# Kernel optimization log

Hardware: AMD Instinct MI355X
Metric: run time of the kernel (lower is better)

The kernel has to match this reference:

```python
import jax, jax.numpy as jnp
import numpy as np

# dims
N, NPG, E, D, ED = 32768, 256, 262144, 128, 32   # nodes, nodes/graph, edges, hidden, edge_dim
HG, CG = 4, 32                                    # GAT heads, per-head channels (HG*CG == D)
HA = 8                                            # global attention heads
DH = D // HA


def _glorot(key, shape):
    fan_in, fan_out = shape[0], shape[-1]
    lim = (6.0 / (fan_in + fan_out)) ** 0.5
    return jax.random.uniform(key, shape, jnp.float32, -lim, lim)


def _ln(x, g, b, eps=1e-5):
    m = x.mean(-1, keepdims=True)
    v = ((x - m) ** 2).mean(-1, keepdims=True)
    return (x - m) * jax.lax.rsqrt(v + eps) * g + b


def setup_inputs() -> dict:
    key = jax.random.key(0)
    ks = jax.random.split(key, 32)
    x = jax.random.normal(ks[0], (N, D), jnp.float32)
    src = jax.random.randint(ks[1], (E,), 0, N, jnp.int32)
    # keep edges intra-graph (graphs are contiguous blocks of NPG nodes)
    dst = (src // NPG) * NPG + jax.random.randint(ks[2], (E,), 0, NPG, jnp.int32)
    edge_index = jnp.stack([src, dst])
    edge_attr = jax.random.normal(ks[3], (E, ED), jnp.float32)
    batch = (jnp.arange(N, dtype=jnp.int32) // NPG)
    return {
        "x": x, "edge_attr": edge_attr,
        # EdgeAwareGATv2 params
        "W_src": _glorot(ks[4], (D, HG * CG)), "W_dst": _glorot(ks[5], (D, HG * CG)),
        "W_edge": _glorot(ks[6], (ED, HG * CG)), "att": _glorot(ks[7], (1, HG, CG)),
        "gat_bias": jnp.zeros((HG * CG,), jnp.float32),
        # GraphMultiHeadAttention params
        "Wq": _glorot(ks[8], (D, D)), "bq": jnp.zeros((D,), jnp.float32),
        "Wk": _glorot(ks[9], (D, D)), "bk": jnp.zeros((D,), jnp.float32),
        "Wv": _glorot(ks[10], (D, D)), "bv": jnp.zeros((D,), jnp.float32),
        "Wo": _glorot(ks[11], (D, D)), "bo": jnp.zeros((D,), jnp.float32),
        "We": _glorot(ks[12], (ED, HA)), "be": jnp.zeros((HA,), jnp.float32),
        # block norms + FFN
        "ln1_g": jnp.ones((D,), jnp.float32), "ln1_b": jnp.zeros((D,), jnp.float32),
        "W1": _glorot(ks[13], (D, 2 * D)), "b1": jnp.zeros((2 * D,), jnp.float32),
        "W2": _glorot(ks[14], (2 * D, D)), "b2": jnp.zeros((D,), jnp.float32),
        "ln2_g": jnp.ones((D,), jnp.float32), "ln2_b": jnp.zeros((D,), jnp.float32),
        "edge_index": edge_index, "batch": batch, "nodes_per_graph": NPG,
    }


def reference(x, edge_attr, W_src, W_dst, W_edge, att, gat_bias,
              Wq, bq, Wk, bk, Wv, bv, Wo, bo, We, be,
              ln1_g, ln1_b, W1, b1, W2, b2, ln2_g, ln2_b,
              edge_index, batch, nodes_per_graph):
    n = int(nodes_per_graph)
    Nn = x.shape[0]
    G = Nn // n
    src, dst = edge_index[0], edge_index[1]

    # ---- local: EdgeAwareGATv2 (segment-softmax attention over incoming edges) ----
    xs = (x @ W_src).reshape(Nn, HG, CG)
    xd = (x @ W_dst).reshape(Nn, HG, CG)
    ef = (edge_attr @ W_edge).reshape(-1, HG, CG)
    msg = jnp.tanh(xs[src] + xd[dst] + ef)                 # [E,HG,CG]
    alpha = (msg * att).sum(-1)                            # [E,HG]
    amax = jax.ops.segment_max(alpha, dst, num_segments=Nn)
    amax = jnp.where(jnp.isfinite(amax), amax, 0.0)        # nodes w/o in-edges
    ex = jnp.exp(alpha - amax[dst])
    den = jax.ops.segment_sum(ex, dst, num_segments=Nn)
    a = ex / (den[dst] + 1e-16)
    h_local = jax.ops.segment_sum(xs[src] * a[:, :, None], dst, num_segments=Nn)
    h_local = h_local.reshape(Nn, HG * CG) + gat_bias

    # ---- global: GraphMultiHeadAttention with edge bias (dense per graph) ----
    q = (x @ Wq + bq).reshape(G, n, HA, DH)
    k = (x @ Wk + bk).reshape(G, n, HA, DH)
    v = (x @ Wv + bv).reshape(G, n, HA, DH)
    attn = jnp.einsum('gnhd,gmhd->gnmh', q, k) * (DH ** -0.5)
    eb = edge_attr @ We + be                               # [E,HA]
    g_id = src // n
    intra = (g_id == dst // n)[:, None]
    attn = attn.at[g_id, src % n, dst % n].add(jnp.where(intra, eb, 0.0))
    attn = jax.nn.softmax(attn, axis=2)                    # softmax over keys (torch dim=1)
    h_attn = jnp.einsum('gnmh,gmhd->gnhd', attn, v).reshape(Nn, D)
    h_attn = h_attn @ Wo + bo

    # ---- GPS combine: residual + norm + FFN ----
    h = _ln(x + h_local + h_attn, ln1_g, ln1_b)
    ffn = jax.nn.gelu(h @ W1 + b1, approximate=False) @ W2 + b2
    return _ln(h + ffn, ln2_g, ln2_b)
```

## Files before the change

### kernel.cpp

```cpp
#include <hip/hip_runtime.h>
#include <hip/hip_bf16.h>

typedef __hip_bfloat16 bf16;
typedef __hip_bfloat162 bf162;
typedef __attribute__((ext_vector_type(8))) short short8;
typedef __attribute__((ext_vector_type(4))) float f32x4;
typedef __attribute__((ext_vector_type(16))) float f32x16;

constexpr int kN   = 32768;
constexpr int kG   = 128;
constexpr int kE   = 262144;
constexpr int kHA  = 8;

__device__ __forceinline__ float b2f(bf16 v){ return __bfloat162float(v); }
__device__ __forceinline__ bf16  f2b(float v){ return __float2bfloat16(v); }
__device__ __forceinline__ float b2f_raw(unsigned short u){
  return __uint_as_float((unsigned)u << 16);
}
__device__ __forceinline__ float tanh_fast(float x){
  float e = __expf(2.f*x);
  return 1.f - 2.f/(e+1.f);
}
__device__ __forceinline__ unsigned int cvtpk_bf16(float lo, float hi){
  unsigned int r;
  asm volatile("v_cvt_pk_bf16_f32 %0, %1, %2" : "=v"(r) : "v"(lo), "v"(hi));
  return r;
}
__device__ __forceinline__ void plane_swap(unsigned int &a, unsigned int &b){
  asm volatile("v_permlane32_swap_b32 %0, %1" : "+v"(a), "+v"(b));
}

__global__ void detect_k(const void* xraw, int* flag){
  const bf16* p = (const bf16*)xraw;
  int good = 0;
  for (int i = threadIdx.x; i < 4096; i += 256){
    float v = fabsf(b2f(p[i]));
    if (v > 0.0009765625f && v < 16.f) good++;
  }
  __shared__ int s[256];
  s[threadIdx.x] = good;
  __syncthreads();
  for (int d = 128; d; d >>= 1){
    if (threadIdx.x < d) s[threadIdx.x] += s[threadIdx.x + d];
    __syncthreads();
  }
  if (threadIdx.x == 0) *flag = (s[0] < 3500) ? 1 : 0;
}

struct ImpEnt { const void* src; void* dst; int n; };
struct ImpArgs { ImpEnt e[23]; };
__global__ __launch_bounds__(256) void import_k(ImpArgs a, const int* __restrict__ flag){
  ImpEnt en = a.e[blockIdx.y];
  const bool f32 = (*flag != 0);
  for (int i = blockIdx.x*256 + threadIdx.x; i < en.n; i += gridDim.x*256){
    float v = f32 ? ((const float*)en.src)[i] : b2f(((const bf16*)en.src)[i]);
    ((float*)en.dst)[i] = v;
  }
}

__global__ __launch_bounds__(256) void repack5_k(const float* __restrict__ W0,
    const float* __restrict__ W1p, const float* __restrict__ W2p,
    const float* __restrict__ W3p, const float* __restrict__ W4p,
    bf16* __restrict__ dst){
  int idx = blockIdx.x*256 + threadIdx.x;
  const float* Ws[5] = {W0, W1p, W2p, W3p, W4p};
  int o = idx >> 14;
  int rem = idx & 16383;
  int j = rem & 7, l = (rem >> 3) & 63, t = rem >> 9;
  int ks = t >> 3, cb = t & 7;
  int k = ks*32 + (l>>4)*8 + j;
  int c = cb*16 + (l&15);
  dst[idx] = f2b(Ws[o][k*128 + c]);
}

struct RepEnt { const float* src; bf16* dst; int total; int ncb_log; int dout; int perm; };
__global__ __launch_bounds__(256) void repack_k(RepEnt e0, RepEnt e1, RepEnt e2, RepEnt e3){
  RepEnt en = (blockIdx.y == 0) ? e0 : (blockIdx.y == 1) ? e1 :
              (blockIdx.y == 2) ? e2 : e3;
  int idx = blockIdx.x*256 + threadIdx.x;
  if (idx >= en.total) return;
  int j = idx & 7, l = (idx >> 3) & 63, t = idx >> 9;
  int ncbm = (1 << en.ncb_log) - 1;
  int ks = t >> en.ncb_log, cb = t & ncbm;
  int k = ks*32 + (l>>4)*8 + j;
  int c = cb*16 + (l&15);
  if (en.perm) c = ((c & 15) << 3) | (c >> 4);
  en.dst[idx] = f2b(en.src[k*en.dout + c]);
}

__global__ __launch_bounds__(256) void gemm5_k(const void* __restrict__ xraw,
    const int* __restrict__ flag,
    const bf16* __restrict__ Wrep, const float* __restrict__ bias5,
    bf16* __restrict__ proj5){
  const int tid = threadIdx.x;
  const int wid = tid >> 6, l = tid & 63;
  const long r0 = (long)blockIdx.x*64 + wid*16;
  const bool f32 = (*flag != 0);
  short8 af[4];
  if (f32){
    const float* fr = (const float*)xraw + (r0 + (l&15))*128;
    #pragma unroll
    for (int ks=0; ks<4; ks++){
      float4 a = *(const float4*)(fr + ks*32 + (l>>4)*8);
      float4 b = *(const float4*)(fr + ks*32 + (l>>4)*8 + 4);
      union{ unsigned int u[4]; short8 s; } c;
      c.u[0]=cvtpk_bf16(a.x,a.y); c.u[1]=cvtpk_bf16(a.z,a.w);
      c.u[2]=cvtpk_bf16(b.x,b.y); c.u[3]=cvtpk_bf16(b.z,b.w);
      af[ks] = c.s;
    }
  } else {
    const short* Arow = (const short*)xraw + (r0 + (l&15))*128;
    #pragma unroll
    for (int ks=0; ks<4; ks++)
      af[ks] = *(const short8*)(Arow + ks*32 + (l>>4)*8);
  }
  const short8* Wp = (const short8*)Wrep;
  const int cc = l & 15, rr = (l >> 4) * 4;
  #pragma unroll 1
  for (int o=0; o<5; o++){
    f32x4 acc[8];
    #pragma unroll
    for (int cb=0; cb<8; cb++) acc[cb] = (f32x4){0.f,0.f,0.f,0.f};
    #pragma unroll
    for (int ks=0; ks<4; ks++){
      #pragma unroll
      for (int cb=0; cb<8; cb++){
        short8 bf = Wp[(o*32 + ks*8 + cb)*64 + l];
        acc[cb] = __builtin_amdgcn_mfma_f32_16x16x32_bf16(af[ks], bf, acc[cb], 0,0,0);
      }
    }
    bf16* outb = proj5 + (long)o*kN*128;
    #pragma unroll
    for (int cb=0; cb<8; cb++){
      float bb = bias5[o*128 + cb*16 + cc];
      #pragma unroll
      for (int r=0; r<4; r++){
        long row = r0 + rr + r;
        outb[row*128 + cb*16 + cc] = f2b(acc[cb][r] + bb);
      }
    }
  }
}

template<int DIN, int DOUT, int EPI>
__global__ __launch_bounds__(256) void gemm_mfma_k(const bf16* __restrict__ A,
    const bf16* __restrict__ Wrep, const float* __restrict__ bias,
    bf16* __restrict__ C){
  constexpr int KS = DIN/32, NCB = DOUT/16;
  const int tid = threadIdx.x;
  const int wid = tid >> 6, l = tid & 63;
  const long r0 = (long)blockIdx.x*64 + wid*16;
  const short* Arow = (const short*)(A + (r0 + (l&15))*(long)DIN);
  short8 af[KS];
  #pragma unroll
  for (int ks=0; ks<KS; ks++)
    af[ks] = *(const short8*)(Arow + ks*32 + (l>>4)*8);
  f32x4 acc[NCB];
  #pragma unroll
  for (int cb=0; cb<NCB; cb++) acc[cb] = (f32x4){0.f,0.f,0.f,0.f};
  const short8* Wp = (const short8*)Wrep;
  #pragma unroll
  for (int ks=0; ks<KS; ks++){
    #pragma unroll
    for (int cb=0; cb<NCB; cb++){
      short8 bf = Wp[(ks*NCB + cb)*64 + l];
      acc[cb] = __builtin_amdgcn_mfma_f32_16x16x32_bf16(af[ks], bf, acc[cb], 0,0,0);
    }
  }
  const int cc = l & 15, rr = (l >> 4) * 4;
  #pragma unroll
  for (int cb=0; cb<NCB; cb++){
    float bb = bias[cb*16 + cc];
    #pragma unroll
    for (int r=0; r<4; r++){
      long row = r0 + rr + r;
      float v = acc[cb][r] + bb;
      if (EPI == 2) v = 0.5f*v*(1.f + erff(v*0.70710678118654752f));
      C[row*DOUT + cb*16 + cc] = f2b(v);
    }
  }
}

__global__ void hist_k(const int* __restrict__ dstA, int* __restrict__ cnt){
  int e = blockIdx.x*256 + threadIdx.x;
  if (e < kE) atomicAdd(&cnt[dstA[e]], 1);
}

__global__ __launch_bounds__(1024) void scan_k(const int* __restrict__ cnt, int* __restrict__ rowptr){
  __shared__ int part[1024];
  const int t = threadIdx.x;
  const int base = t*32;
  int s = 0;
  #pragma unroll
  for (int i=0;i<32;i++) s += cnt[base+i];
  part[t] = s;
  __syncthreads();
  for (int d=1; d<1024; d<<=1){
    int v = (t>=d) ? part[t-d] : 0;
    __syncthreads();
    part[t] += v;
    __syncthreads();
  }
  int run = (t==0) ? 0 : part[t-1];
  for (int i=0;i<32;i++){ rowptr[base+i] = run; run += cnt[base+i]; }
  if (t == 1023) rowptr[kN] = run;
}

__global__ void scatter_k(const int* __restrict__ dstA, const int* __restrict__ rowptr,
                          int* __restrict__ cursor, int* __restrict__ eidx){
  int e = blockIdx.x*256 + threadIdx.x;
  if (e < kE){
    int d = dstA[e];
    int p = atomicAdd(&cursor[d], 1);
    eidx[rowptr[d]+p] = e;
  }
}

__global__ __launch_bounds__(256) void edge3_k(const void* __restrict__ ea_raw,
    const int* __restrict__ flag,
    const int* __restrict__ eidx, const int* __restrict__ srcA,
    const int* __restrict__ dstA,
    const bf16* __restrict__ xs, const bf16* __restrict__ xd,
    const bf16* __restrict__ WeR_edge,
    const float* __restrict__ We_f, const float* __restrict__ att_f,
    const float* __restrict__ be_f,
    float* __restrict__ expal_t, float* __restrict__ ebuf_t,
    unsigned short* __restrict__ epack, int* __restrict__ src_t){
  __shared__ unsigned short sxd[64*136];
  __shared__ float sWe[256];
  __shared__ float sBe[8];
  __shared__ int   sEid[64], sSrc[64], sDst[64];
  __shared__ float sAlphaF[64*4];
  const int tid = threadIdx.x;
  const int w = tid >> 6, l = tid & 63;
  const long t0 = (long)blockIdx.x * 64;
  const bool f32 = (*flag != 0);

  if (tid < 64){
    int e = eidx[t0 + tid];
    int s = srcA[e], d = dstA[e];
    sEid[tid] = e; sSrc[tid] = s; sDst[tid] = d;
    src_t[t0 + tid] = s;
    epack[t0 + tid] = (unsigned short)(((s & 255) << 8) | (d & 255));
  }
  if (tid < 256) sWe[tid] = We_f[tid];
  if (tid >= 128 && tid < 136) sBe[tid-128] = be_f[tid-128];
  __syncthreads();

  short8 af;
  {
    long eoff = (long)sEid[w*16 + (l&15)]*32 + (l>>4)*8;
    if (f32){
      const float* er = (const float*)ea_raw + eoff;
      float4 a = *(const float4*)er;
      float4 b = *(const float4*)(er + 4);
      union{ unsigned int u[4]; short8 s; } c;
      c.u[0]=cvtpk_bf16(a.x,a.y); c.u[1]=cvtpk_bf16(a.z,a.w);
      c.u[2]=cvtpk_bf16(b.x,b.y); c.u[3]=cvtpk_bf16(b.z,b.w);
      af = c.s;
    } else {
      af = *(const short8*)((const short*)ea_raw + eoff);
    }
  }
  short8 wb[8];
  #pragma unroll
  for (int cb=0; cb<8; cb++)
    wb[cb] = *(const short8*)((const short*)WeR_edge + (cb*64 + l)*8);

  {
    const int c0 = (tid & 31) * 4;
    const int rb = tid >> 5;
    const unsigned short* xsu = (const unsigned short*)xs;
    const unsigned short* xdu = (const unsigned short*)xd;
    #pragma unroll 4
    for (int p = 0; p < 8; p++){
      int row = p*8 + rb;
      long s = sSrc[row], dd = sDst[row];
      ushort4 a = *(const ushort4*)(xsu + s*128 + c0);
      ushort4 b = *(const ushort4*)(xdu + dd*128 + c0);
      unsigned int lo = cvtpk_bf16(b2f_raw(a.x)+b2f_raw(b.x), b2f_raw(a.y)+b2f_raw(b.y));
      unsigned int hi = cvtpk_bf16(b2f_raw(a.z)+b2f_raw(b.z), b2f_raw(a.w)+b2f_raw(b.w));
      *(uint2*)&sxd[row*136 + c0] = (uint2){lo, hi};
    }
  }

  f32x4 acc[8];
  #pragma unroll
  for (int cb=0; cb<8; cb++)
    acc[cb] = __builtin_amdgcn_mfma_f32_16x16x32_bf16(af, wb[cb],
                (f32x4){0.f,0.f,0.f,0.f}, 0,0,0);

  {
    int e_eb = tid >> 2, h0 = (tid & 3) * 2;
    long ebase = (long)sEid[e_eb]*32;
    float a0 = sBe[h0], a1 = sBe[h0+1];
    #pragma unroll
    for (int dq=0; dq<8; dq++){
      float f0,f1,f2,f3;
      if (f32){
        float4 u = *(const float4*)((const float*)ea_raw + ebase + dq*4);
        f0=u.x; f1=u.y; f2=u.z; f3=u.w;
      } else {
        ushort4 u = *(const ushort4*)((const unsigned short*)ea_raw + ebase + dq*4);
        f0=b2f_raw(u.x); f1=b2f_raw(u.y); f2=b2f_raw(u.z); f3=b2f_raw(u.w);
      }
      a0 += f0*sWe[(dq*4+0)*8 + h0]   + f1*sWe[(dq*4+1)*8 + h0]
          + f2*sWe[(dq*4+2)*8 + h0]   + f3*sWe[(dq*4+3)*8 + h0];
      a1 += f0*sWe[(dq*4+0)*8 + h0+1] + f1*sWe[(dq*4+1)*8 + h0+1]
          + f2*sWe[(dq*4+2)*8 + h0+1] + f3*sWe[(dq*4+3)*8 + h0+1];
    }
    ebuf_t[(long)h0*kE     + t0 + e_eb] = a0;
    ebuf_t[(long)(h0+1)*kE + t0 + e_eb] = a1;
  }
  __syncthreads();

  const int c15 = l & 15;
  float4 at0 = *(const float4*)(att_f + c15*8);
  float4 at1 = *(const float4*)(att_f + c15*8 + 4);
  const float attv[8] = {at0.x,at0.y,at0.z,at0.w, at1.x,at1.y,at1.z,at1.w};
  #pragma unroll
  for (int r=0; r<4; r++){
    int e_l = w*16 + (l>>4)*4 + r;
    union{ short8 s8; unsigned short u[8]; } sx;
    sx.s8 = *(short8*)&sxd[e_l*136 + c15*8];
    float hsum = 0.f;
    #pragma unroll
    for (int cb=0; cb<8; cb++){
      float v = acc[cb][r] + b2f_raw(sx.u[cb]);
      hsum += tanh_fast(v) * attv[cb];
    }
    hsum += __shfl_xor(hsum,1);
    hsum += __shfl_xor(hsum,2);
    if ((c15 & 3) == 0) sAlphaF[e_l*4 + (c15>>2)] = __expf(hsum);
  }
  __syncthreads();
  if (tid < 64)
    *(float4*)&expal_t[(t0 + tid)*4] = *(float4*)&sAlphaF[tid*4];
}

__global__ __launch_bounds__(256) void gat_agg_k(const float* __restrict__ expal,
    const int* __restrict__ rowptr, const int* __restrict__ src_t,
    const bf16* __restrict__ xs, const float* __restrict__ gatb_f,
    bf16* __restrict__ h_local){
  const int tid = threadIdx.x;
  const int grp = tid >> 5;
  const int l   = tid & 31;
  const int v   = blockIdx.x*8 + grp;
  const int c0  = l*4;
  const int head = l >> 3;
  const int beg = rowptr[v], end = rowptr[v+1];
  float den = 0.f, o0 = 0.f, o1 = 0.f, o2 = 0.f, o3 = 0.f;
  const unsigned short* xsu = (const unsigned short*)xs;
  for (int t = beg; t < end; t++){
    float w = expal[(long)t*4 + head];
    long s = src_t[t];
    ushort4 a = *(const ushort4*)(xsu + s*128 + c0);
    den += w;
    o0 += w*b2f_raw(a.x); o1 += w*b2f_raw(a.y);
    o2 += w*b2f_raw(a.z); o3 += w*b2f_raw(a.w);
  }
  float inv = 1.f/(den + 1e-16f);
  float4 gb = *(const float4*)(gatb_f + c0);
  unsigned int lo = cvtpk_bf16(o0*inv + gb.x, o1*inv + gb.y);
  unsigned int hi = cvtpk_bf16(o2*inv + gb.z, o3*inv + gb.w);
  *(uint2*)&((unsigned short*)h_local)[(long)v*128 + c0] = (uint2){lo, hi};
}

__global__ __launch_bounds__(512, 6) void attn2_k(const bf16* __restrict__ qb,
    const bf16* __restrict__ kb, const bf16* __restrict__ vb,
    const float* __restrict__ ebuf_t, const unsigned short* __restrict__ epack,
    const int* __restrict__ rowptr, bf16* __restrict__ hattn){
  __shared__ short Vf[16*64*8];
  __shared__ float sb[256*33];
  const int bid = blockIdx.x;
  const int h = (bid >> 3) >> 4;
  const int g = (((bid >> 3) & 15) << 3) | (bid & 7);
  const int tid = threadIdx.x;
  const int w = tid >> 6, l = tid & 63;
  const int q31 = l & 31, hi = l >> 5;
  const int nbase = g << 8;

  for (int s2 = tid; s2 < 1024; s2 += 512){
    int f = s2 >> 6, ll = s2 & 63;
    int keyb = (f>>1)*32 + (f&1)*16 + ((ll>>5)*8);
    int d = ll & 15;
    short tmp[8];
    #pragma unroll
    for (int j=0;j<8;j++)
      tmp[j] = ((const short*)vb)[((long)(nbase + keyb + j))*128 + h*16 + d];
    *(short8*)&Vf[s2*8] = *(short8*)tmp;
  }
  for (int i = tid; i < 256*33; i += 512) sb[i] = 0.f;
  short8 qf = *(const short8*)((const short*)qb + ((long)(nbase + w*32 + q31))*128 + h*16 + hi*8);
  __syncthreads();

  float m = -1e30f, lsum = 0.f;
  f32x16 oacc = {0.f,0.f,0.f,0.f,0.f,0.f,0.f,0.f,0.f,0.f,0.f,0.f,0.f,0.f,0.f,0.f};
  #pragma unroll 1
  for (int kt = 0; kt < 8; kt++){
    int rb = rowptr[nbase + kt*32];
    int re = rowptr[nbase + kt*32 + 32];
    for (int t = rb + tid; t < re; t += 512){
      unsigned int p = epack[t];
      atomicAdd(&sb[(p>>8)*33 + (p&31)], ebuf_t[(long)h*kE + t]);
    }
    __syncthreads();
    short8 af = *(const short8*)((const short*)kb +
                 ((long)(nbase + kt*32 + q31))*128 + h*16 + hi*8);
    f32x16 acc = {0.f,0.f,0.f,0.f,0.f,0.f,0.f,0.f,0.f,0.f,0.f,0.f,0.f,0.f,0.f,0.f};
    acc = __builtin_amdgcn_mfma_f32_32x32x16_bf16(af, qf, acc, 0, 0, 0);
    float s[16];
    float* brow = &sb[(w*32 + q31)*33];
    #pragma unroll
    for (int r=0;r<16;r++){
      int krow = (r&3) + 8*(r>>2) + 4*hi;
      s[r] = acc[r]*0.25f + brow[krow];
      brow[krow] = 0.f;
    }
    __syncthreads();
    float tmax = s[0];
    #pragma unroll
    for (int r=1;r<16;r++) tmax = fmaxf(tmax, s[r]);
    tmax = fmaxf(tmax, __shfl_xor(tmax, 32));
    float mn = fmaxf(m, tmax);
    float corrq = __expf(m - mn);
    m = mn;
    float psum = 0.f;
    #pragma unroll
    for (int r=0;r<16;r++){ s[r] = __expf(s[r] - m); psum += s[r]; }
    lsum = lsum*corrq + psum;
    #pragma unroll
    for (int r=0;r<16;r++){
      int qrow = (r&3) + 8*(r>>2) + 4*hi;
      oacc[r] *= __shfl(corrq, qrow);
    }
    unsigned int a  = cvtpk_bf16(s[0],  s[1]);
    unsigned int b  = cvtpk_bf16(s[2],  s[3]);
    unsigned int c  = cvtpk_bf16(s[4],  s[5]);
    unsigned int d  = cvtpk_bf16(s[6],  s[7]);
    unsigned int e  = cvtpk_bf16(s[8],  s[9]);
    unsigned int f  = cvtpk_bf16(s[10], s[11]);
    unsigned int g2 = cvtpk_bf16(s[12], s[13]);
    unsigned int h2 = cvtpk_bf16(s[14], s[15]);
    plane_swap(a, c); plane_swap(b, d); plane_swap(e, g2); plane_swap(f, h2);
    union { unsigned int u[4]; short8 s8; } A1, A2;
    A1.u[0]=a; A1.u[1]=b; A1.u[2]=c; A1.u[3]=d;
    A2.u[0]=e; A2.u[1]=f; A2.u[2]=g2; A2.u[3]=h2;
    short8 v1 = *(short8*)&Vf[((kt*2+0)*64 + l)*8];
    short8 v2 = *(short8*)&Vf[((kt*2+1)*64 + l)*8];
    oacc = __builtin_amdgcn_mfma_f32_32x32x16_bf16(A1.s8, v1, oacc, 0,0,0);
    oacc = __builtin_amdgcn_mfma_f32_32x32x16_bf16(A2.s8, v2, oacc, 0,0,0);
  }
  lsum += __shfl_xor(lsum, 32);
  float linv = 1.f / lsum;
  #pragma unroll
  for (int r=0;r<16;r++){
    int qrow = (r&3) + 8*(r>>2) + 4*hi;
    float li = __shfl(linv, qrow);
    float ov = oacc[r]*li;
    if (q31 < 16)
      hattn[((long)(nbase + w*32 + qrow))*128 + h*16 + q31] = f2b(ov);
  }
}

__global__ __launch_bounds__(256) void combine_ln_k(const void* __restrict__ a,
    const bf16* __restrict__ b, const bf16* __restrict__ c3,
    const float* __restrict__ g, const float* __restrict__ bb,
    void* __restrict__ outp, const int* __restrict__ flag,
    int a_raw, int is_final){
  const int tid = threadIdx.x;
  const int lane = tid & 63;
  const long row = (long)blockIdx.x*4 + (tid>>6);
  const long base = row*128;
  float a0, a1;
  if (a_raw && (*flag)){
    const float* ap = (const float*)a;
    a0 = ap[base+lane]; a1 = ap[base+lane+64];
  } else {
    const bf16* ap = (const bf16*)a;
    a0 = b2f(ap[base+lane]); a1 = b2f(ap[base+lane+64]);
  }
  float v0 = a0 + b2f(b[base+lane]);
  float v1 = a1 + b2f(b[base+lane+64]);
  if (c3){ v0 += b2f(c3[base+lane]); v1 += b2f(c3[base+lane+64]); }
  float s = v0 + v1;
  #pragma unroll
  for (int o=1; o<64; o<<=1) s += __shfl_xor(s, o);
  float mean = s * (1.f/128.f);
  float d0 = v0 - mean, d1 = v1 - mean;
  float q = d0*d0 + d1*d1;
  #pragma unroll
  for (int o=1; o<64; o<<=1) q += __shfl_xor(q, o);
  float r = rsqrtf(q*(1.f/128.f) + 1e-5f);
  float r0v = d0*r*g[lane]    + bb[lane];
  float r1v = d1*r*g[lane+64] + bb[lane+64];
  if (is_final && (*flag)){
    float* o = (float*)outp;
    o[base+lane]    = r0v;
    o[base+lane+64] = r1v;
  } else {
    bf16* o = (bf16*)outp;
    o[base+lane]    = f2b(r0v);
    o[base+lane+64] = f2b(r1v);
  }
}

extern "C" void kernel_launch(void* const* d_in, const int* in_sizes, int n_in,
                              void* d_out, int out_size, void* d_ws, size_t ws_size,
                              hipStream_t stream){
  const void* x_raw   = d_in[0];
  const void* ea_raw  = d_in[1];
  const int*  ei      = (const int*)d_in[25];
  const int* srcA = ei;
  const int* dstA = ei + kE;

  char* ws = (char*)d_ws;
  size_t off = 0;
  auto alloc = [&](size_t bytes)->void*{
    void* p = ws + off;
    off = (off + bytes + 255) & ~(size_t)255;
    return p;
  };
  int*   flag    = (int*)alloc(4);
  float* Wsrc_f  = (float*)alloc(16384*4);
  float* Wdst_f  = (float*)alloc(16384*4);
  float* Wedge_f = (float*)alloc(4096*4);
  float* att_f   = (float*)alloc(128*4);
  float* gatb_f  = (float*)alloc(128*4);
  float* Wq_f    = (float*)alloc(16384*4);
  float* Wk_f    = (float*)alloc(16384*4);
  float* Wv_f    = (float*)alloc(16384*4);
  float* Wo_f    = (float*)alloc(16384*4);
  float* bo_f    = (float*)alloc(128*4);
  float* We_f    = (float*)alloc(256*4);
  float* be_f    = (float*)alloc(8*4);
  float* ln1g_f  = (float*)alloc(128*4);
  float* ln1b_f  = (float*)alloc(128*4);
  float* W1_f    = (float*)alloc(32768*4);
  float* b1_f    = (float*)alloc(256*4);
  float* W2_f    = (float*)alloc(32768*4);
  float* b2_f    = (float*)alloc(128*4);
  float* ln2g_f  = (float*)alloc(128*4);
  float* ln2b_f  = (float*)alloc(128*4);
  float* bias5   = (float*)alloc(640*4);
  bf16*  Wrep5   = (bf16*)alloc((size_t)5*16384*2);
  bf16*  WoR     = (bf16*)alloc((size_t)16384*2);
  bf16*  W1R     = (bf16*)alloc((size_t)32768*2);
  bf16*  W2R     = (bf16*)alloc((size_t)32768*2);
  bf16*  WeR     = (bf16*)alloc((size_t)4096*2);
  bf16*  proj5   = (bf16*)alloc((size_t)5*kN*128*2);
  bf16* xs   = proj5;
  bf16* xd   = proj5 + (size_t)kN*128;
  bf16* qb   = proj5 + (size_t)2*kN*128;
  bf16* kbuf = proj5 + (size_t)3*kN*128;
  bf16* vbuf = proj5 + (size_t)4*kN*128;
  int* cnt        = (int*)alloc((size_t)2*kN*4);
  int* cursor     = cnt + kN;
  int* rowptr     = (int*)alloc((size_t)(kN+1)*4);
  int* eidx       = (int*)alloc((size_t)kE*4);
  unsigned short* epack = (unsigned short*)alloc((size_t)kE*2);
  float* ebuf_t   = (float*)alloc((size_t)8*kE*4);
  float* expal_t  = (float*)alloc((size_t)kE*4*4);
  int*   src_t    = (int*)alloc((size_t)kE*4);
  bf16* h_local   = (bf16*)alloc((size_t)kN*128*2);
  bf16* hattn_pre = (bf16*)alloc((size_t)kN*128*2);
  bf16* h_attn    = (bf16*)alloc((size_t)kN*128*2);
  bf16* hbuf      = (bf16*)alloc((size_t)kN*128*2);
  bf16* tbuf      = (bf16*)alloc((size_t)kN*256*2);
  bf16* f2buf     = (bf16*)alloc((size_t)kN*128*2);
  (void)ws_size; (void)in_sizes; (void)n_in; (void)out_size;

  dim3 b256(256);

  detect_k<<<1, b256, 0, stream>>>(x_raw, flag);
  hipMemsetAsync(bias5, 0, 256*4, stream);
  hipMemsetAsync(cnt, 0, (size_t)2*kN*4, stream);

  hist_k<<<kE/256, b256, 0, stream>>>(dstA, cnt);
  scan_k<<<1, 1024, 0, stream>>>(cnt, rowptr);
  scatter_k<<<kE/256, b256, 0, stream>>>(dstA, rowptr, cursor, eidx);

  ImpArgs ia;
  const void* srcs[23] = {d_in[2], d_in[3], d_in[4], d_in[5], d_in[6],
                          d_in[7], d_in[8], d_in[9], d_in[10], d_in[11], d_in[12],
                          d_in[13], d_in[14], d_in[15], d_in[16], d_in[17], d_in[18],
                          d_in[19], d_in[20], d_in[21], d_in[22], d_in[23], d_in[24]};
  void* dsts[23] = {Wsrc_f, Wdst_f, Wedge_f, att_f, gatb_f,
                    Wq_f, bias5+256, Wk_f, bias5+384, Wv_f, bias5+512,
                    Wo_f, bo_f, We_f, be_f, ln1g_f, ln1b_f,
                    W1_f, b1_f, W2_f, b2_f, ln2g_f, ln2b_f};
  int ns[23] = {16384, 16384, 4096, 128, 128,
                16384, 128, 16384, 128, 16384, 128,
                16384, 128, 256, 8, 128, 128,
                32768, 256, 32768, 128, 128, 128};
  for (int i=0;i<23;i++){ ia.e[i].src=srcs[i]; ia.e[i].dst=dsts[i]; ia.e[i].n=ns[i]; }
  import_k<<<dim3(64,23), b256, 0, stream>>>(ia, flag);

  repack5_k<<<(5*16384)/256, b256, 0, stream>>>(Wsrc_f, Wdst_f, Wq_f, Wk_f, Wv_f, Wrep5);
  RepEnt ro{Wo_f, WoR, 16384, 3, 128, 0};
  RepEnt r1{W1_f, W1R, 32768, 4, 256, 0};
  RepEnt r2{W2_f, W2R, 32768, 3, 128, 0};
  RepEnt re{Wedge_f, WeR, 4096, 3, 128, 1};
  repack_k<<<dim3(128,4), b256, 0, stream>>>(ro, r1, r2, re);

  gemm5_k<<<kN/64, b256, 0, stream>>>(x_raw, flag, Wrep5, bias5, proj5);

  edge3_k<<<kE/64, b256, 0, stream>>>(ea_raw, flag, eidx, srcA, dstA, xs, xd,
                                      WeR, We_f, att_f, be_f,
                                      expal_t, ebuf_t, epack, src_t);

  gat_agg_k<<<kN/8, b256, 0, stream>>>(expal_t, rowptr, src_t, xs, gatb_f, h_local);

  attn2_k<<<kG*kHA, dim3(512), 0, stream>>>(qb, kbuf, vbuf, ebuf_t, epack, rowptr, hattn_pre);
  gemm_mfma_k<128,128,1><<<kN/64, b256, 0, stream>>>(hattn_pre, WoR, bo_f, h_attn);

  combine_ln_k<<<kN/4, b256, 0, stream>>>(x_raw, h_local, h_attn, ln1g_f, ln1b_f,
                                          hbuf, flag, 1, 0);

  gemm_mfma_k<128,256,2><<<kN/64, b256, 0, stream>>>(hbuf, W1R, b1_f, tbuf);
  gemm_mfma_k<256,128,1><<<kN/64, b256, 0, stream>>>(tbuf, W2R, b2_f, f2buf);

  combine_ln_k<<<kN/4, b256, 0, stream>>>(hbuf, f2buf, nullptr, ln2g_f, ln2b_f,
                                          d_out, flag, 0, 1);
}
```

Before: 261.0 us.

## Compute edge bias via MFMA and gather xs/xd directly in edge kernel

The edge-bias projection (edge_attr @ We + be) is now done with an extra MFMA on the already-loaded bf16 edge fragment, using a new zero-padded repacked We weight. This replaces the scalar FP32 loop that re-read edge_attr from global memory. The shared-memory staging of xs+xd rows is removed: each lane gathers the src and dst rows straight into registers and adds them in FP32. Block indices in edge3_k and gat_agg_k are also remapped so consecutive launched blocks are spread across the grid, likely to balance XCD/L2 locality. The edge bias now uses bf16 inputs instead of FP32, which changes rounding.

```diff
diff --git a/kernel.cpp b/kernel.cpp
--- a/kernel.cpp
+++ b/kernel.cpp
@@ -73,18 +73,25 @@
   dst[idx] = f2b(Ws[o][k*128 + c]);
 }
 
-struct RepEnt { const float* src; bf16* dst; int total; int ncb_log; int dout; int perm; };
-__global__ __launch_bounds__(256) void repack_k(RepEnt e0, RepEnt e1, RepEnt e2, RepEnt e3){
+struct RepEnt { const float* src; bf16* dst; int total; int ncb_log; int dout; int mode; };
+__global__ __launch_bounds__(256) void repack_k(RepEnt e0, RepEnt e1, RepEnt e2,
+                                                RepEnt e3, RepEnt e4){
   RepEnt en = (blockIdx.y == 0) ? e0 : (blockIdx.y == 1) ? e1 :
-              (blockIdx.y == 2) ? e2 : e3;
+              (blockIdx.y == 2) ? e2 : (blockIdx.y == 3) ? e3 : e4;
   int idx = blockIdx.x*256 + threadIdx.x;
   if (idx >= en.total) return;
   int j = idx & 7, l = (idx >> 3) & 63, t = idx >> 9;
+  if (en.mode == 2){
+    int k = (l>>4)*8 + j;
+    int c = l & 15;
+    en.dst[idx] = (c < 8) ? f2b(en.src[k*8 + c]) : f2b(0.f);
+    return;
+  }
   int ncbm = (1 << en.ncb_log) - 1;
   int ks = t >> en.ncb_log, cb = t & ncbm;
   int k = ks*32 + (l>>4)*8 + j;
   int c = cb*16 + (l&15);
-  if (en.perm) c = ((c & 15) << 3) | (c >> 4);
+  if (en.mode == 1) c = ((c & 15) << 3) | (c >> 4);
   en.dst[idx] = f2b(en.src[k*en.dout + c]);
 }
 
@@ -222,18 +229,17 @@
     const int* __restrict__ dstA,
     const bf16* __restrict__ xs, const bf16* __restrict__ xd,
     const bf16* __restrict__ WeR_edge,
-    const float* __restrict__ We_f, const float* __restrict__ att_f,
-    const float* __restrict__ be_f,
+    const bf16* __restrict__ WeR_eb,
+    const float* __restrict__ att_f, const float* __restrict__ be_f,
     float* __restrict__ expal_t, float* __restrict__ ebuf_t,
     unsigned short* __restrict__ epack, int* __restrict__ src_t){
-  __shared__ unsigned short sxd[64*136];
-  __shared__ float sWe[256];
-  __shared__ float sBe[8];
-  __shared__ int   sEid[64], sSrc[64], sDst[64];
+  __shared__ int sEid[64], sSrc[64], sDst[64];
   __shared__ float sAlphaF[64*4];
   const int tid = threadIdx.x;
   const int w = tid >> 6, l = tid & 63;
-  const long t0 = (long)blockIdx.x * 64;
+  const int p = blockIdx.x;
+  const int bid = (p & 7) * (gridDim.x >> 3) + (p >> 3);
+  const long t0 = (long)bid * 64;
   const bool f32 = (*flag != 0);
 
   if (tid < 64){
@@ -243,8 +249,6 @@
     src_t[t0 + tid] = s;
     epack[t0 + tid] = (unsigned short)(((s & 255) << 8) | (d & 255));
   }
-  if (tid < 256) sWe[tid] = We_f[tid];
-  if (tid >= 128 && tid < 136) sBe[tid-128] = be_f[tid-128];
   __syncthreads();
 
   short8 af;
@@ -262,76 +266,46 @@
       af = *(const short8*)((const short*)ea_raw + eoff);
     }
   }
-  short8 wb[8];
-  #pragma unroll
-  for (int cb=0; cb<8; cb++)
-    wb[cb] = *(const short8*)((const short*)WeR_edge + (cb*64 + l)*8);
-
+
+  f32x4 acc[8], acc_eb;
+  #pragma unroll
+  for (int cb=0; cb<8; cb++){
+    short8 wb = *(const short8*)((const short*)WeR_edge + (cb*64 + l)*8);
+    acc[cb] = __builtin_amdgcn_mfma_f32_16x16x32_bf16(af, wb,
+                (f32x4){0.f,0.f,0.f,0.f}, 0,0,0);
+  }
   {
-    const int c0 = (tid & 31) * 4;
-    const int rb = tid >> 5;
-    const unsigned short* xsu = (const unsigned short*)xs;
-    const unsigned short* xdu = (const unsigned short*)xd;
-    #pragma unroll 4
-    for (int p = 0; p < 8; p++){
-      int row = p*8 + rb;
-      long s = sSrc[row], dd = sDst[row];
-      ushort4 a = *(const ushort4*)(xsu + s*128 + c0);
-      ushort4 b = *(const ushort4*)(xdu + dd*128 + c0);
-      unsigned int lo = cvtpk_bf16(b2f_raw(a.x)+b2f_raw(b.x), b2f_raw(a.y)+b2f_raw(b.y));
-      unsigned int hi = cvtpk_bf16(b2f_raw(a.z)+b2f_raw(b.z), b2f_raw(a.w)+b2f_raw(b.w));
-      *(uint2*)&sxd[row*136 + c0] = (uint2){lo, hi};
-    }
-  }
-
-  f32x4 acc[8];
-  #pragma unroll
-  for (int cb=0; cb<8; cb++)
-    acc[cb] = __builtin_amdgcn_mfma_f32_16x16x32_bf16(af, wb[cb],
+    short8 wbe = *(const short8*)((const short*)WeR_eb + l*8);
+    acc_eb = __builtin_amdgcn_mfma_f32_16x16x32_bf16(af, wbe,
                 (f32x4){0.f,0.f,0.f,0.f}, 0,0,0);
-
-  {
-    int e_eb = tid >> 2, h0 = (tid & 3) * 2;
-    long ebase = (long)sEid[e_eb]*32;
-    float a0 = sBe[h0], a1 = sBe[h0+1];
-    #pragma unroll
-    for (int dq=0; dq<8; dq++){
-      float f0,f1,f2,f3;
-      if (f32){
-        float4 u = *(const float4*)((const float*)ea_raw + ebase + dq*4);
-        f0=u.x; f1=u.y; f2=u.z; f3=u.w;
-      } else {
-        ushort4 u = *(const ushort4*)((const unsigned short*)ea_raw + ebase + dq*4);
-        f0=b2f_raw(u.x); f1=b2f_raw(u.y); f2=b2f_raw(u.z); f3=b2f_raw(u.w);
-      }
-      a0 += f0*sWe[(dq*4+0)*8 + h0]   + f1*sWe[(dq*4+1)*8 + h0]
-          + f2*sWe[(dq*4+2)*8 + h0]   + f3*sWe[(dq*4+3)*8 + h0];
-      a1 += f0*sWe[(dq*4+0)*8 + h0+1] + f1*sWe[(dq*4+1)*8 + h0+1]
-          + f2*sWe[(dq*4+2)*8 + h0+1] + f3*sWe[(dq*4+3)*8 + h0+1];
-    }
-    ebuf_t[(long)h0*kE     + t0 + e_eb] = a0;
-    ebuf_t[(long)(h0+1)*kE + t0 + e_eb] = a1;
-  }
-  __syncthreads();
+  }
 
   const int c15 = l & 15;
+  const float be_v = be_f[c15 & 7];
   float4 at0 = *(const float4*)(att_f + c15*8);
   float4 at1 = *(const float4*)(att_f + c15*8 + 4);
   const float attv[8] = {at0.x,at0.y,at0.z,at0.w, at1.x,at1.y,at1.z,at1.w};
+  union U8 { short8 s8; unsigned short u[8]; };
+  U8 gx[4], gd[4];
   #pragma unroll
   for (int r=0; r<4; r++){
     int e_l = w*16 + (l>>4)*4 + r;
-    union{ short8 s8; unsigned short u[8]; } sx;
-    sx.s8 = *(short8*)&sxd[e_l*136 + c15*8];
+    gx[r].s8 = *(const short8*)((const short*)xs + (long)sSrc[e_l]*128 + c15*8);
+    gd[r].s8 = *(const short8*)((const short*)xd + (long)sDst[e_l]*128 + c15*8);
+  }
+  #pragma unroll
+  for (int r=0; r<4; r++){
+    int e_l = w*16 + (l>>4)*4 + r;
     float hsum = 0.f;
     #pragma unroll
     for (int cb=0; cb<8; cb++){
-      float v = acc[cb][r] + b2f_raw(sx.u[cb]);
+      float v = acc[cb][r] + b2f_raw(gx[r].u[cb]) + b2f_raw(gd[r].u[cb]);
       hsum += tanh_fast(v) * attv[cb];
     }
     hsum += __shfl_xor(hsum,1);
     hsum += __shfl_xor(hsum,2);
     if ((c15 & 3) == 0) sAlphaF[e_l*4 + (c15>>2)] = __expf(hsum);
+    if (c15 < 8) ebuf_t[(long)c15*kE + t0 + e_l] = acc_eb[r] + be_v;
   }
   __syncthreads();
   if (tid < 64)
@@ -345,7 +319,9 @@
   const int tid = threadIdx.x;
   const int grp = tid >> 5;
   const int l   = tid & 31;
-  const int v   = blockIdx.x*8 + grp;
+  const int p   = blockIdx.x;
+  const int bid = (p & 7) * (gridDim.x >> 3) + (p >> 3);
+  const int v   = bid*8 + grp;
   const int c0  = l*4;
   const int head = l >> 3;
   const int beg = rowptr[v], end = rowptr[v+1];
@@ -548,6 +524,7 @@
   bf16*  W1R     = (bf16*)alloc((size_t)32768*2);
   bf16*  W2R     = (bf16*)alloc((size_t)32768*2);
   bf16*  WeR     = (bf16*)alloc((size_t)4096*2);
+  bf16*  WeRb    = (bf16*)alloc((size_t)512*2);
   bf16*  proj5   = (bf16*)alloc((size_t)5*kN*128*2);
   bf16* xs   = proj5;
   bf16* xd   = proj5 + (size_t)kN*128;
@@ -601,12 +578,13 @@
   RepEnt r1{W1_f, W1R, 32768, 4, 256, 0};
   RepEnt r2{W2_f, W2R, 32768, 3, 128, 0};
   RepEnt re{Wedge_f, WeR, 4096, 3, 128, 1};
-  repack_k<<<dim3(128,4), b256, 0, stream>>>(ro, r1, r2, re);
+  RepEnt rb{We_f, WeRb, 512, 0, 8, 2};
+  repack_k<<<dim3(128,5), b256, 0, stream>>>(ro, r1, r2, re, rb);
 
   gemm5_k<<<kN/64, b256, 0, stream>>>(x_raw, flag, Wrep5, bias5, proj5);
 
   edge3_k<<<kE/64, b256, 0, stream>>>(ea_raw, flag, eidx, srcA, dstA, xs, xd,
-                                      WeR, We_f, att_f, be_f,
+                                      WeR, WeRb, att_f, be_f,
                                       expal_t, ebuf_t, epack, src_t);
 
   gat_agg_k<<<kN/8, b256, 0, stream>>>(expal_t, rowptr, src_t, xs, gatb_f, h_local);
```

Measured after the change: 234.9 us. -10.0%, faster.
